# Kernel tuning notes

Measured on AMD Instinct MI355X. Metric: run time of the kernel, lower is better.

Reference implementation:

```python
import jax, jax.numpy as jnp
import numpy as np

B, S, D = 4, 4096, 1024
H, HID, ATT = 16, 64, 64


def setup_inputs() -> dict:
    key = jax.random.key(0)
    ks = jax.random.split(key, 7)
    sc = 0.02
    return {
        "x": jax.random.normal(ks[0], (B, S, D), dtype=jnp.float32),
        "Wq": jax.random.normal(ks[1], (D, H * HID), dtype=jnp.float32) * sc,
        "bq": jnp.zeros((H * HID,), dtype=jnp.float32),
        "Wk": jax.random.normal(ks[2], (D, H * HID), dtype=jnp.float32) * sc,
        "bk": jnp.zeros((H * HID,), dtype=jnp.float32),
        "Wv": jax.random.normal(ks[3], (D, H * ATT), dtype=jnp.float32) * sc,
        "bv": jnp.zeros((H * ATT,), dtype=jnp.float32),
    }


def reference(x, Wq, bq, Wk, bk, Wv, bv):
    b, s, _ = x.shape
    q = (x @ Wq + bq).reshape(b, s, H, HID)
    k = (x @ Wk + bk).reshape(b, s, H, HID)
    v = (x @ Wv + bv).reshape(b, s, H, ATT)
    # attention across the head axis: [B,S,H,H] scores per token
    scores = jnp.einsum("bsid,bsjd->bsij", q, k) / np.sqrt(HID).astype(np.float32)
    probs = jax.nn.softmax(scores, axis=-1)
    ctx = jnp.einsum("bsij,bsja->bsia", probs, v)
    return ctx.reshape(b, s, H * ATT)
```

## Files before the change

### kernel.cpp

```cpp
#include <hip/hip_runtime.h>


#define AS1 __attribute__((address_space(1)))
#define AS3 __attribute__((address_space(3)))

typedef __bf16 bf16x8 __attribute__((ext_vector_type(8)));
typedef float f32x4 __attribute__((ext_vector_type(4)));
typedef float f32x16 __attribute__((ext_vector_type(16)));
typedef unsigned short u16x8 __attribute__((ext_vector_type(8)));

static constexpr int MTOK = 16384;
static constexpr int N3   = 3072;
static constexpr int KD   = 1024;
static constexpr int NT   = KD / 64;

__device__ __forceinline__ unsigned short f2bf(float f) {
  unsigned u = __float_as_uint(f);
  unsigned r = u + 0x7FFFu + ((u >> 16) & 1u);
  return (unsigned short)(r >> 16);
}
__device__ __forceinline__ float bf2f(unsigned short s) {
  return __uint_as_float(((unsigned)s) << 16);
}

__device__ __forceinline__ void gload_lds16(const void* g, void* lds_uniform) {
  __builtin_amdgcn_global_load_lds((const AS1 void*)g, (AS3 void*)lds_uniform, 16, 0, 0);
}

__global__ __launch_bounds__(256) void cvt_x_kernel(const float* __restrict__ x,
                                                    unsigned short* __restrict__ xb) {
  int i = blockIdx.x * 256 + threadIdx.x;
  const float4* p = (const float4*)x;
  float4 a = p[2 * i], b = p[2 * i + 1];
  u16x8 o;
  o[0] = f2bf(a.x); o[1] = f2bf(a.y); o[2] = f2bf(a.z); o[3] = f2bf(a.w);
  o[4] = f2bf(b.x); o[5] = f2bf(b.y); o[6] = f2bf(b.z); o[7] = f2bf(b.w);
  *((u16x8*)xb + i) = o;
}

__global__ __launch_bounds__(256) void prep_w_kernel(const float* __restrict__ Wq,
                                                     const float* __restrict__ Wk,
                                                     const float* __restrict__ Wv,
                                                     const float* __restrict__ bq,
                                                     const float* __restrict__ bk,
                                                     const float* __restrict__ bv,
                                                     unsigned short* __restrict__ WT,
                                                     float* __restrict__ bcat) {
  __shared__ float tile[32][33];
  int kt = blockIdx.x * 32;
  int nt = blockIdx.y * 32;
  const float* W; const float* bias; int nb;
  if (nt < 1024)      { W = Wq; bias = bq; nb = nt; }
  else if (nt < 2048) { W = Wk; bias = bk; nb = nt - 1024; }
  else                { W = Wv; bias = bv; nb = nt - 2048; }
  int tx = threadIdx.x & 31, ty = threadIdx.x >> 5;
#pragma unroll
  for (int it = 0; it < 4; ++it) {
    int kk = it * 8 + ty;
    tile[kk][tx] = W[(size_t)(kt + kk) * 1024 + nb + tx];
  }
  __syncthreads();
#pragma unroll
  for (int it = 0; it < 4; ++it) {
    int nn = it * 8 + ty;
    WT[(size_t)(nt + nn) * 1024 + kt + tx] = f2bf(tile[tx][nn]);
  }
  if (blockIdx.x == 0 && threadIdx.x < 32)
    bcat[nt + threadIdx.x] = bias[nb + threadIdx.x];
}

__global__ __launch_bounds__(512, 2) void gemm_qkv_kernel(const unsigned short* __restrict__ A,
                                                          const unsigned short* __restrict__ Bt,
                                                          const float* __restrict__ bias,
                                                          unsigned short* __restrict__ C) {
  __shared__ __align__(16) unsigned short lds[65536];
  const int tid  = threadIdx.x;
  const int lane = tid & 63;
  const int wave = tid >> 6;
  const int wm = wave >> 2, wn = wave & 3;
  const int m0 = blockIdx.x * 256;
  const int n0 = blockIdx.y * 256;

  const int srow = tid >> 2;
  const int sc   = ((tid & 3) ^ ((srow >> 1) & 3)) * 8;
  const size_t asrc0 = (size_t)(m0 + srow) * KD + sc;
  const size_t asrc1 = (size_t)(m0 + 128 + srow) * KD + sc;
  const size_t bsrc0 = (size_t)(n0 + srow) * KD + sc;
  const size_t bsrc1 = (size_t)(n0 + 128 + srow) * KD + sc;

  int aoff[4][2], boff[2][2];
#pragma unroll
  for (int m = 0; m < 4; ++m) {
    int row = wm * 128 + m * 32 + (lane & 31);
#pragma unroll
    for (int ks = 0; ks < 2; ++ks) {
      int pc = (ks * 2 + (lane >> 5)) ^ ((row >> 1) & 3);
      aoff[m][ks] = row * 32 + pc * 8;
    }
  }
#pragma unroll
  for (int n = 0; n < 2; ++n) {
    int row = wn * 64 + n * 32 + (lane & 31);
#pragma unroll
    for (int ks = 0; ks < 2; ++ks) {
      int pc = (ks * 2 + (lane >> 5)) ^ ((row >> 1) & 3);
      boff[n][ks] = 8192 + row * 32 + pc * 8;
    }
  }

  f32x16 acc[4][2] = {};

#define STAGE(T, S)                                                            \
  do {                                                                         \
    unsigned short* dst = lds + ((T) & 1) * 32768 + (S) * 16384 + tid * 8;     \
    const int kk = (T) * 64 + (S) * 32;                                        \
    gload_lds16(A  + asrc0 + kk, dst);                                         \
    gload_lds16(A  + asrc1 + kk, dst + 4096);                                  \
    gload_lds16(Bt + bsrc0 + kk, dst + 8192);                                  \
    gload_lds16(Bt + bsrc1 + kk, dst + 12288);                                 \
  } while (0)

#define PHASE(T, S, DOSTAGE, ST, SS)                                           \
  do {                                                                         \
    const unsigned short* bufp = lds + ((T) & 1) * 32768 + (S) * 16384;        \
    bf16x8 af[4][2], bfr[2][2];                                                \
    _Pragma("unroll") for (int m = 0; m < 4; ++m)                              \
      _Pragma("unroll") for (int ks = 0; ks < 2; ++ks)                         \
        af[m][ks] = *(const bf16x8*)(bufp + aoff[m][ks]);                      \
    _Pragma("unroll") for (int n = 0; n < 2; ++n)                              \
      _Pragma("unroll") for (int ks = 0; ks < 2; ++ks)                         \
        bfr[n][ks] = *(const bf16x8*)(bufp + boff[n][ks]);                     \
    if (DOSTAGE) { STAGE(ST, SS); }                                            \
    asm volatile("s_waitcnt lgkmcnt(0)" ::: "memory");                         \
    __builtin_amdgcn_sched_barrier(0);                                         \
    __builtin_amdgcn_s_setprio(1);                                             \
    _Pragma("unroll") for (int ks = 0; ks < 2; ++ks)                           \
      _Pragma("unroll") for (int m = 0; m < 4; ++m)                            \
        _Pragma("unroll") for (int n = 0; n < 2; ++n)                          \
          acc[m][n] = __builtin_amdgcn_mfma_f32_32x32x16_bf16(af[m][ks],       \
                          bfr[n][ks], acc[m][n], 0, 0, 0);                     \
    __builtin_amdgcn_s_setprio(0);                                             \
  } while (0)

#define SYNC(VM)                                                               \
  do {                                                                         \
    asm volatile("s_waitcnt vmcnt(" #VM ")" ::: "memory");                     \
    __builtin_amdgcn_s_barrier();                                              \
    __builtin_amdgcn_sched_barrier(0);                                         \
  } while (0)

  STAGE(0, 0); STAGE(0, 1); STAGE(1, 0);

#pragma unroll 1
  for (int t = 0; t < NT - 2; ++t) {
    SYNC(8); PHASE(t, 0, true, t + 1, 1);
    SYNC(8); PHASE(t, 1, true, t + 2, 0);
  }
  SYNC(8); PHASE(NT - 2, 0, true, NT - 1, 1);
  SYNC(8); PHASE(NT - 2, 1, false, 0, 0);
  SYNC(4); PHASE(NT - 1, 0, false, 0, 0);
  SYNC(0); PHASE(NT - 1, 1, false, 0, 0);
#undef STAGE
#undef PHASE
#undef SYNC

#pragma unroll
  for (int n = 0; n < 2; ++n) {
    int col = n0 + wn * 64 + n * 32 + (lane & 31);
    float bvv = bias[col];
#pragma unroll
    for (int m = 0; m < 4; ++m) {
      int rowb = m0 + wm * 128 + m * 32 + 4 * (lane >> 5);
#pragma unroll
      for (int r = 0; r < 16; ++r) {
        int row = rowb + (r & 3) + 8 * (r >> 2);
        C[(size_t)row * N3 + col] = f2bf(acc[m][n][r] + bvv);
      }
    }
  }
}

__global__ __launch_bounds__(256) void attn_kernel(const unsigned short* __restrict__ qkv,
                                                   float* __restrict__ out) {
  __shared__ float p_lds[4][16][17];
  const int tid = threadIdx.x;
  const int lane = tid & 63;
  const int w = tid >> 6;
  const size_t token = (size_t)blockIdx.x * 4 + w;
  const unsigned short* rowp = qkv + token * N3;
  const int head = lane & 15;
  const int chunk = lane >> 4;

  const int o = head * 64 + chunk * 8;
  bf16x8 q0 = *(const bf16x8*)(rowp + o);
  bf16x8 q1 = *(const bf16x8*)(rowp + o + 32);
  bf16x8 k0 = *(const bf16x8*)(rowp + 1024 + o);
  bf16x8 k1 = *(const bf16x8*)(rowp + 1024 + o + 32);
  f32x4 c = {0.f, 0.f, 0.f, 0.f};
  c = __builtin_amdgcn_mfma_f32_16x16x32_bf16(q0, k0, c, 0, 0, 0);
  c = __builtin_amdgcn_mfma_f32_16x16x32_bf16(q1, k1, c, 0, 0, 0);

#pragma unroll
  for (int r = 0; r < 4; ++r) {
    float s = c[r] * 0.125f;
    float m = s;
#pragma unroll
    for (int off = 1; off < 16; off <<= 1) m = fmaxf(m, __shfl_xor(m, off, 64));
    float e = __expf(s - m);
    float sum = e;
#pragma unroll
    for (int off = 1; off < 16; off <<= 1) sum += __shfl_xor(sum, off, 64);
    p_lds[w][chunk * 4 + r][head] = e / sum;
  }
  __syncthreads();

  const int i = lane >> 2;
  const int ab = lane & 3;
  const unsigned short* vbase = rowp + 2048 + ab * 16;
  float accv[16];
#pragma unroll
  for (int cc = 0; cc < 16; ++cc) accv[cc] = 0.f;
#pragma unroll
  for (int j = 0; j < 16; ++j) {
    float pij = p_lds[w][i][j];
    u16x8 v0 = *(const u16x8*)(vbase + j * 64);
    u16x8 v1 = *(const u16x8*)(vbase + j * 64 + 8);
#pragma unroll
    for (int cc = 0; cc < 8; ++cc) accv[cc] += pij * bf2f(v0[cc]);
#pragma unroll
    for (int cc = 0; cc < 8; ++cc) accv[8 + cc] += pij * bf2f(v1[cc]);
  }
  float* op = out + token * 1024 + i * 64 + ab * 16;
#pragma unroll
  for (int cc = 0; cc < 16; cc += 4) {
    f32x4 v = {accv[cc], accv[cc + 1], accv[cc + 2], accv[cc + 3]};
    *(f32x4*)(op + cc) = v;
  }
}

extern "C" void kernel_launch(void* const* d_in, const int* in_sizes, int n_in,
                              void* d_out, int out_size, void* d_ws, size_t ws_size,
                              hipStream_t stream) {
  const float* x  = (const float*)d_in[0];
  const float* Wq = (const float*)d_in[1];
  const float* bq = (const float*)d_in[2];
  const float* Wk = (const float*)d_in[3];
  const float* bk = (const float*)d_in[4];
  const float* Wv = (const float*)d_in[5];
  const float* bv = (const float*)d_in[6];
  float* out = (float*)d_out;

  char* ws = (char*)d_ws;
  unsigned short* xb   = (unsigned short*)ws;
  unsigned short* WT   = (unsigned short*)(ws + 33554432);
  float*          bcat = (float*)(ws + 39845888);
  unsigned short* qkv  = (unsigned short*)(ws + 39858176);

  cvt_x_kernel<<<dim3((MTOK * KD / 8) / 256), 256, 0, stream>>>(x, xb);
  prep_w_kernel<<<dim3(32, 96), 256, 0, stream>>>(Wq, Wk, Wv, bq, bk, bv, WT, bcat);
  gemm_qkv_kernel<<<dim3(MTOK / 256, N3 / 256), 512, 0, stream>>>(xb, WT, bcat, qkv);
  attn_kernel<<<dim3(MTOK / 4), 256, 0, stream>>>(qkv, out);
}
```

Measured before the change: 171.9 us.

## Store GEMM tiles in MFMA-fragment order and use a four-slot ring buffer

The QKV GEMM now loads A and B so that each lane's 16-byte chunk lands in LDS exactly where the MFMA fragment read expects it. This replaces the XOR-swizzled row layout with contiguous per-lane reads, aiming to remove bank conflicts and address arithmetic. The pipeline also moves from a double buffer with two sub-stages to a four-slot ring of 32-wide K slices, with prefetch three slices ahead. The global loads now read only 16 bytes per row per lane chunk at strided rows, which may reduce coalescing.

```diff
diff --git a/kernel.cpp b/kernel.cpp
--- a/kernel.cpp
+++ b/kernel.cpp
@@ -12,7 +12,6 @@
 static constexpr int MTOK = 16384;
 static constexpr int N3   = 3072;
 static constexpr int KD   = 1024;
-static constexpr int NT   = KD / 64;
 
 __device__ __forceinline__ unsigned short f2bf(float f) {
   unsigned u = __float_as_uint(f);
@@ -23,8 +22,8 @@
   return __uint_as_float(((unsigned)s) << 16);
 }
 
-__device__ __forceinline__ void gload_lds16(const void* g, void* lds_uniform) {
-  __builtin_amdgcn_global_load_lds((const AS1 void*)g, (AS3 void*)lds_uniform, 16, 0, 0);
+__device__ __forceinline__ void gload_lds16(const void* g, void* lds_ptr) {
+  __builtin_amdgcn_global_load_lds((const AS1 void*)g, (AS3 void*)lds_ptr, 16, 0, 0);
 }
 
 __global__ __launch_bounds__(256) void cvt_x_kernel(const float* __restrict__ x,
@@ -81,48 +80,36 @@
   const int m0 = blockIdx.x * 256;
   const int n0 = blockIdx.y * 256;
 
-  const int srow = tid >> 2;
-  const int sc   = ((tid & 3) ^ ((srow >> 1) & 3)) * 8;
-  const size_t asrc0 = (size_t)(m0 + srow) * KD + sc;
-  const size_t asrc1 = (size_t)(m0 + 128 + srow) * KD + sc;
-  const size_t bsrc0 = (size_t)(n0 + srow) * KD + sc;
-  const size_t bsrc1 = (size_t)(n0 + 128 + srow) * KD + sc;
+  const size_t afrow = (size_t)(m0 + wave * 32 + (lane & 31)) * KD + ((lane >> 5) * 8);
+  const size_t bfrow = (size_t)(n0 + wave * 32 + (lane & 31)) * KD + ((lane >> 5) * 8);
+  const int dbase = wave * 1024 + lane * 8;
 
   int aoff[4][2], boff[2][2];
 #pragma unroll
-  for (int m = 0; m < 4; ++m) {
-    int row = wm * 128 + m * 32 + (lane & 31);
-#pragma unroll
-    for (int ks = 0; ks < 2; ++ks) {
-      int pc = (ks * 2 + (lane >> 5)) ^ ((row >> 1) & 3);
-      aoff[m][ks] = row * 32 + pc * 8;
-    }
-  }
-#pragma unroll
-  for (int n = 0; n < 2; ++n) {
-    int row = wn * 64 + n * 32 + (lane & 31);
-#pragma unroll
-    for (int ks = 0; ks < 2; ++ks) {
-      int pc = (ks * 2 + (lane >> 5)) ^ ((row >> 1) & 3);
-      boff[n][ks] = 8192 + row * 32 + pc * 8;
-    }
-  }
+  for (int m = 0; m < 4; ++m)
+#pragma unroll
+    for (int ks = 0; ks < 2; ++ks)
+      aoff[m][ks] = ((wm * 4 + m) * 2 + ks) * 512 + lane * 8;
+#pragma unroll
+  for (int n = 0; n < 2; ++n)
+#pragma unroll
+    for (int ks = 0; ks < 2; ++ks)
+      boff[n][ks] = 8192 + ((wn * 2 + n) * 2 + ks) * 512 + lane * 8;
 
   f32x16 acc[4][2] = {};
 
-#define STAGE(T, S)                                                            \
+#define STAGE(SLOT, KK)                                                        \
   do {                                                                         \
-    unsigned short* dst = lds + ((T) & 1) * 32768 + (S) * 16384 + tid * 8;     \
-    const int kk = (T) * 64 + (S) * 32;                                        \
-    gload_lds16(A  + asrc0 + kk, dst);                                         \
-    gload_lds16(A  + asrc1 + kk, dst + 4096);                                  \
-    gload_lds16(Bt + bsrc0 + kk, dst + 8192);                                  \
-    gload_lds16(Bt + bsrc1 + kk, dst + 12288);                                 \
+    unsigned short* da = lds + (SLOT) * 16384 + dbase;                         \
+    gload_lds16(A  + afrow + (KK),      da);                                   \
+    gload_lds16(A  + afrow + (KK) + 16, da + 512);                             \
+    gload_lds16(Bt + bfrow + (KK),      da + 8192);                            \
+    gload_lds16(Bt + bfrow + (KK) + 16, da + 8704);                            \
   } while (0)
 
-#define PHASE(T, S, DOSTAGE, ST, SS)                                           \
+#define PH(SLOT, DOSTAGE, KSTG)                                                \
   do {                                                                         \
-    const unsigned short* bufp = lds + ((T) & 1) * 32768 + (S) * 16384;        \
+    const unsigned short* bufp = lds + (SLOT) * 16384;                         \
     bf16x8 af[4][2], bfr[2][2];                                                \
     _Pragma("unroll") for (int m = 0; m < 4; ++m)                              \
       _Pragma("unroll") for (int ks = 0; ks < 2; ++ks)                         \
@@ -130,7 +117,7 @@
     _Pragma("unroll") for (int n = 0; n < 2; ++n)                              \
       _Pragma("unroll") for (int ks = 0; ks < 2; ++ks)                         \
         bfr[n][ks] = *(const bf16x8*)(bufp + boff[n][ks]);                     \
-    if (DOSTAGE) { STAGE(ST, SS); }                                            \
+    if (DOSTAGE) { STAGE(((SLOT) + 3) & 3, KSTG); }                            \
     asm volatile("s_waitcnt lgkmcnt(0)" ::: "memory");                         \
     __builtin_amdgcn_sched_barrier(0);                                         \
     __builtin_amdgcn_s_setprio(1);                                             \
@@ -149,19 +136,22 @@
     __builtin_amdgcn_sched_barrier(0);                                         \
   } while (0)
 
-  STAGE(0, 0); STAGE(0, 1); STAGE(1, 0);
+  STAGE(0, 0); STAGE(1, 32); STAGE(2, 64);
 
 #pragma unroll 1
-  for (int t = 0; t < NT - 2; ++t) {
-    SYNC(8); PHASE(t, 0, true, t + 1, 1);
-    SYNC(8); PHASE(t, 1, true, t + 2, 0);
-  }
-  SYNC(8); PHASE(NT - 2, 0, true, NT - 1, 1);
-  SYNC(8); PHASE(NT - 2, 1, false, 0, 0);
-  SYNC(4); PHASE(NT - 1, 0, false, 0, 0);
-  SYNC(0); PHASE(NT - 1, 1, false, 0, 0);
+  for (int t = 0; t < 7; ++t) {
+    const int kb = t * 128;
+    SYNC(8); PH(0, true, kb + 96);
+    SYNC(8); PH(1, true, kb + 128);
+    SYNC(8); PH(2, true, kb + 160);
+    SYNC(8); PH(3, true, kb + 192);
+  }
+  SYNC(8); PH(0, true, 992);
+  SYNC(8); PH(1, false, 0);
+  SYNC(4); PH(2, false, 0);
+  SYNC(0); PH(3, false, 0);
 #undef STAGE
-#undef PHASE
+#undef PH
 #undef SYNC
 
 #pragma unroll
```

After: 180.8 us. 1.05x slower.

## Replace 4-slot LDS pipeline with 2-slot double buffer to halve GEMM LDS

Applied to the files above, without the earlier changes.

The QKV GEMM's four-slot LDS ring, which kept three 32-wide K stages in flight, becomes a simple two-slot double buffer. Each iteration prefetches only the next stage, runs its MFMAs, then waits for all outstanding loads and barriers. This halves shared memory from 128KB to 64KB per block, so two 512-thread blocks can fit on a CU as the launch bounds intend. The trade-off is only one stage of load latency hiding per block, plus a full vmcnt drain every iteration, relying on the co-resident block to cover memory stalls.

```diff
diff --git a/kernel.cpp b/kernel.cpp
--- a/kernel.cpp
+++ b/kernel.cpp
@@ -12,7 +12,6 @@
 static constexpr int MTOK = 16384;
 static constexpr int N3   = 3072;
 static constexpr int KD   = 1024;
-static constexpr int NT   = KD / 64;
 
 __device__ __forceinline__ unsigned short f2bf(float f) {
   unsigned u = __float_as_uint(f);
@@ -23,8 +22,8 @@
   return __uint_as_float(((unsigned)s) << 16);
 }
 
-__device__ __forceinline__ void gload_lds16(const void* g, void* lds_uniform) {
-  __builtin_amdgcn_global_load_lds((const AS1 void*)g, (AS3 void*)lds_uniform, 16, 0, 0);
+__device__ __forceinline__ void gload_lds16(const void* g, void* lds_ptr) {
+  __builtin_amdgcn_global_load_lds((const AS1 void*)g, (AS3 void*)lds_ptr, 16, 0, 0);
 }
 
 __global__ __launch_bounds__(256) void cvt_x_kernel(const float* __restrict__ x,
@@ -73,7 +72,7 @@
                                                           const unsigned short* __restrict__ Bt,
                                                           const float* __restrict__ bias,
                                                           unsigned short* __restrict__ C) {
-  __shared__ __align__(16) unsigned short lds[65536];
+  __shared__ __align__(16) unsigned short lds[32768];
   const int tid  = threadIdx.x;
   const int lane = tid & 63;
   const int wave = tid >> 6;
@@ -110,59 +109,57 @@
 
   f32x16 acc[4][2] = {};
 
-#define STAGE(T, S)                                                            \
+#define STAGE(SLOT, KK)                                                        \
   do {                                                                         \
-    unsigned short* dst = lds + ((T) & 1) * 32768 + (S) * 16384 + tid * 8;     \
-    const int kk = (T) * 64 + (S) * 32;                                        \
-    gload_lds16(A  + asrc0 + kk, dst);                                         \
-    gload_lds16(A  + asrc1 + kk, dst + 4096);                                  \
-    gload_lds16(Bt + bsrc0 + kk, dst + 8192);                                  \
-    gload_lds16(Bt + bsrc1 + kk, dst + 12288);                                 \
+    unsigned short* dst = lds + (SLOT) * 16384 + tid * 8;                      \
+    gload_lds16(A  + asrc0 + (KK), dst);                                       \
+    gload_lds16(A  + asrc1 + (KK), dst + 4096);                                \
+    gload_lds16(Bt + bsrc0 + (KK), dst + 8192);                                \
+    gload_lds16(Bt + bsrc1 + (KK), dst + 12288);                               \
   } while (0)
 
-#define PHASE(T, S, DOSTAGE, ST, SS)                                           \
-  do {                                                                         \
-    const unsigned short* bufp = lds + ((T) & 1) * 32768 + (S) * 16384;        \
-    bf16x8 af[4][2], bfr[2][2];                                                \
-    _Pragma("unroll") for (int m = 0; m < 4; ++m)                              \
-      _Pragma("unroll") for (int ks = 0; ks < 2; ++ks)                         \
-        af[m][ks] = *(const bf16x8*)(bufp + aoff[m][ks]);                      \
-    _Pragma("unroll") for (int n = 0; n < 2; ++n)                              \
-      _Pragma("unroll") for (int ks = 0; ks < 2; ++ks)                         \
-        bfr[n][ks] = *(const bf16x8*)(bufp + boff[n][ks]);                     \
-    if (DOSTAGE) { STAGE(ST, SS); }                                            \
-    asm volatile("s_waitcnt lgkmcnt(0)" ::: "memory");                         \
-    __builtin_amdgcn_sched_barrier(0);                                         \
-    __builtin_amdgcn_s_setprio(1);                                             \
-    _Pragma("unroll") for (int ks = 0; ks < 2; ++ks)                           \
-      _Pragma("unroll") for (int m = 0; m < 4; ++m)                            \
-        _Pragma("unroll") for (int n = 0; n < 2; ++n)                          \
-          acc[m][n] = __builtin_amdgcn_mfma_f32_32x32x16_bf16(af[m][ks],       \
-                          bfr[n][ks], acc[m][n], 0, 0, 0);                     \
-    __builtin_amdgcn_s_setprio(0);                                             \
-  } while (0)
-
-#define SYNC(VM)                                                               \
-  do {                                                                         \
-    asm volatile("s_waitcnt vmcnt(" #VM ")" ::: "memory");                     \
-    __builtin_amdgcn_s_barrier();                                              \
-    __builtin_amdgcn_sched_barrier(0);                                         \
-  } while (0)
-
-  STAGE(0, 0); STAGE(0, 1); STAGE(1, 0);
+  STAGE(0, 0);
+  asm volatile("s_waitcnt vmcnt(0)" ::: "memory");
+  __builtin_amdgcn_s_barrier();
 
 #pragma unroll 1
-  for (int t = 0; t < NT - 2; ++t) {
-    SYNC(8); PHASE(t, 0, true, t + 1, 1);
-    SYNC(8); PHASE(t, 1, true, t + 2, 0);
-  }
-  SYNC(8); PHASE(NT - 2, 0, true, NT - 1, 1);
-  SYNC(8); PHASE(NT - 2, 1, false, 0, 0);
-  SYNC(4); PHASE(NT - 1, 0, false, 0, 0);
-  SYNC(0); PHASE(NT - 1, 1, false, 0, 0);
+  for (int s = 0; s < 32; ++s) {
+    const unsigned short* bufp = lds + (s & 1) * 16384;
+    bf16x8 af[4][2], bfr[2][2];
+#pragma unroll
+    for (int m = 0; m < 4; ++m)
+#pragma unroll
+      for (int ks = 0; ks < 2; ++ks)
+        af[m][ks] = *(const bf16x8*)(bufp + aoff[m][ks]);
+#pragma unroll
+    for (int n = 0; n < 2; ++n)
+#pragma unroll
+      for (int ks = 0; ks < 2; ++ks)
+        bfr[n][ks] = *(const bf16x8*)(bufp + boff[n][ks]);
+    if (s < 31) {
+      unsigned short* dst = lds + ((s + 1) & 1) * 16384 + tid * 8;
+      const int kk = (s + 1) * 32;
+      gload_lds16(A  + asrc0 + kk, dst);
+      gload_lds16(A  + asrc1 + kk, dst + 4096);
+      gload_lds16(Bt + bsrc0 + kk, dst + 8192);
+      gload_lds16(Bt + bsrc1 + kk, dst + 12288);
+    }
+    __builtin_amdgcn_s_setprio(1);
+#pragma unroll
+    for (int ks = 0; ks < 2; ++ks)
+#pragma unroll
+      for (int m = 0; m < 4; ++m)
+#pragma unroll
+        for (int n = 0; n < 2; ++n)
+          acc[m][n] = __builtin_amdgcn_mfma_f32_32x32x16_bf16(af[m][ks], bfr[n][ks],
+                                                              acc[m][n], 0, 0, 0);
+    __builtin_amdgcn_s_setprio(0);
+    if (s < 31) {
+      asm volatile("s_waitcnt vmcnt(0)" ::: "memory");
+      __builtin_amdgcn_s_barrier();
+    }
+  }
 #undef STAGE
-#undef PHASE
-#undef SYNC
 
 #pragma unroll
   for (int n = 0; n < 2; ++n) {
```

After: 178.6 us. 3.9% more time.

## Software-pipeline LDS fragment reads against MFMAs with a four-slot ring buffer

Applied to the files above, without the earlier changes.

Reworks the GEMM main loop into a four-slot LDS ring with ping-pong register fragments. LDS reads for the next K-step are issued before the current step's MFMAs, so the explicit lgkmcnt(0) wait and sched_barrier in front of the MFMAs are gone. The aim is to hide LDS read latency behind matrix math. In exchange it doubles the fragment registers and relies on the compiler to place waitcnts correctly, which could cost occupancy or ordering control.

```diff
diff --git a/kernel.cpp b/kernel.cpp
--- a/kernel.cpp
+++ b/kernel.cpp
@@ -12,7 +12,6 @@
 static constexpr int MTOK = 16384;
 static constexpr int N3   = 3072;
 static constexpr int KD   = 1024;
-static constexpr int NT   = KD / 64;
 
 __device__ __forceinline__ unsigned short f2bf(float f) {
   unsigned u = __float_as_uint(f);
@@ -23,8 +22,8 @@
   return __uint_as_float(((unsigned)s) << 16);
 }
 
-__device__ __forceinline__ void gload_lds16(const void* g, void* lds_uniform) {
-  __builtin_amdgcn_global_load_lds((const AS1 void*)g, (AS3 void*)lds_uniform, 16, 0, 0);
+__device__ __forceinline__ void gload_lds16(const void* g, void* lds_ptr) {
+  __builtin_amdgcn_global_load_lds((const AS1 void*)g, (AS3 void*)lds_ptr, 16, 0, 0);
 }
 
 __global__ __launch_bounds__(256) void cvt_x_kernel(const float* __restrict__ x,
@@ -109,36 +108,36 @@
   }
 
   f32x16 acc[4][2] = {};
-
-#define STAGE(T, S)                                                            \
-  do {                                                                         \
-    unsigned short* dst = lds + ((T) & 1) * 32768 + (S) * 16384 + tid * 8;     \
-    const int kk = (T) * 64 + (S) * 32;                                        \
-    gload_lds16(A  + asrc0 + kk, dst);                                         \
-    gload_lds16(A  + asrc1 + kk, dst + 4096);                                  \
-    gload_lds16(Bt + bsrc0 + kk, dst + 8192);                                  \
-    gload_lds16(Bt + bsrc1 + kk, dst + 12288);                                 \
-  } while (0)
-
-#define PHASE(T, S, DOSTAGE, ST, SS)                                           \
-  do {                                                                         \
-    const unsigned short* bufp = lds + ((T) & 1) * 32768 + (S) * 16384;        \
-    bf16x8 af[4][2], bfr[2][2];                                                \
+  bf16x8 afP[4][2], bfP[2][2], afQ[4][2], bfQ[2][2];
+
+#define STAGE(SLOT, KK)                                                        \
+  do {                                                                         \
+    unsigned short* dst = lds + (SLOT) * 16384 + tid * 8;                      \
+    gload_lds16(A  + asrc0 + (KK), dst);                                       \
+    gload_lds16(A  + asrc1 + (KK), dst + 4096);                                \
+    gload_lds16(Bt + bsrc0 + (KK), dst + 8192);                                \
+    gload_lds16(Bt + bsrc1 + (KK), dst + 12288);                               \
+  } while (0)
+
+#define READF(AF, BF, SLOT)                                                    \
+  do {                                                                         \
+    const unsigned short* bufp = lds + (SLOT) * 16384;                         \
     _Pragma("unroll") for (int m = 0; m < 4; ++m)                              \
       _Pragma("unroll") for (int ks = 0; ks < 2; ++ks)                         \
-        af[m][ks] = *(const bf16x8*)(bufp + aoff[m][ks]);                      \
+        AF[m][ks] = *(const bf16x8*)(bufp + aoff[m][ks]);                      \
     _Pragma("unroll") for (int n = 0; n < 2; ++n)                              \
       _Pragma("unroll") for (int ks = 0; ks < 2; ++ks)                         \
-        bfr[n][ks] = *(const bf16x8*)(bufp + boff[n][ks]);                     \
-    if (DOSTAGE) { STAGE(ST, SS); }                                            \
-    asm volatile("s_waitcnt lgkmcnt(0)" ::: "memory");                         \
-    __builtin_amdgcn_sched_barrier(0);                                         \
+        BF[n][ks] = *(const bf16x8*)(bufp + boff[n][ks]);                      \
+  } while (0)
+
+#define MFMAC(AF, BF)                                                          \
+  do {                                                                         \
     __builtin_amdgcn_s_setprio(1);                                             \
     _Pragma("unroll") for (int ks = 0; ks < 2; ++ks)                           \
       _Pragma("unroll") for (int m = 0; m < 4; ++m)                            \
         _Pragma("unroll") for (int n = 0; n < 2; ++n)                          \
-          acc[m][n] = __builtin_amdgcn_mfma_f32_32x32x16_bf16(af[m][ks],       \
-                          bfr[n][ks], acc[m][n], 0, 0, 0);                     \
+          acc[m][n] = __builtin_amdgcn_mfma_f32_32x32x16_bf16(AF[m][ks],       \
+                          BF[n][ks], acc[m][n], 0, 0, 0);                      \
     __builtin_amdgcn_s_setprio(0);                                             \
   } while (0)
 
@@ -146,22 +145,27 @@
   do {                                                                         \
     asm volatile("s_waitcnt vmcnt(" #VM ")" ::: "memory");                     \
     __builtin_amdgcn_s_barrier();                                              \
-    __builtin_amdgcn_sched_barrier(0);                                         \
-  } while (0)
-
-  STAGE(0, 0); STAGE(0, 1); STAGE(1, 0);
+  } while (0)
+
+  STAGE(0, 0); STAGE(1, 32); STAGE(2, 64);
+  SYNC(4);
+  READF(afP, bfP, 0);
 
 #pragma unroll 1
-  for (int t = 0; t < NT - 2; ++t) {
-    SYNC(8); PHASE(t, 0, true, t + 1, 1);
-    SYNC(8); PHASE(t, 1, true, t + 2, 0);
-  }
-  SYNC(8); PHASE(NT - 2, 0, true, NT - 1, 1);
-  SYNC(8); PHASE(NT - 2, 1, false, 0, 0);
-  SYNC(4); PHASE(NT - 1, 0, false, 0, 0);
-  SYNC(0); PHASE(NT - 1, 1, false, 0, 0);
+  for (int t = 0; t < 7; ++t) {
+    const int kb = t * 128;
+    READF(afQ, bfQ, 1); STAGE(3, kb + 96);  MFMAC(afP, bfP); SYNC(4);
+    READF(afP, bfP, 2); STAGE(0, kb + 128); MFMAC(afQ, bfQ); SYNC(4);
+    READF(afQ, bfQ, 3); STAGE(1, kb + 160); MFMAC(afP, bfP); SYNC(4);
+    READF(afP, bfP, 0); STAGE(2, kb + 192); MFMAC(afQ, bfQ); SYNC(4);
+  }
+  READF(afQ, bfQ, 1); STAGE(3, 992); MFMAC(afP, bfP); SYNC(4);
+  READF(afP, bfP, 2);                MFMAC(afQ, bfQ); SYNC(0);
+  READF(afQ, bfQ, 3);                MFMAC(afP, bfP); SYNC(0);
+                                     MFMAC(afQ, bfQ);
 #undef STAGE
-#undef PHASE
+#undef READF
+#undef MFMAC
 #undef SYNC
 
 #pragma unroll
```

Measured after the change: 215.6 us. +25.5%, slower.
